# Optimization experiments

Hardware: AMD Instinct MI355X
Metric: run time of the kernel (lower is better)

Reference implementation:

```python
import jax, jax.numpy as jnp
import numpy as np

NUM_TOKENS = 16384
HIDDEN = 4096
NUM_EXPERTS = 256
TOP_K = 8
N_GROUP = 8
TOPK_GROUP = 4
NORM_TOPK_PROB = True
ROUTED_SCALING_FACTOR = 1.0


def setup_inputs() -> dict:
    key = jax.random.key(0)
    k1, k2, k3 = jax.random.split(key, 3)
    hidden_states = jax.random.normal(k1, (NUM_TOKENS, HIDDEN), dtype=jnp.float32)
    weight = jax.random.normal(k2, (NUM_EXPERTS, HIDDEN), dtype=jnp.float32) * (HIDDEN ** -0.5)
    e_score_correction_bias = jax.random.normal(k3, (NUM_EXPERTS,), dtype=jnp.float32) * 0.01
    return {"hidden_states": hidden_states, "weight": weight,
            "e_score_correction_bias": e_score_correction_bias}


def reference(hidden_states, weight, e_score_correction_bias):
    num_tokens = hidden_states.shape[0]
    # router logits: [T, E]
    logits = jnp.einsum('th,eh->te', hidden_states.astype(jnp.float32),
                        weight.astype(jnp.float32))
    scores = jax.nn.sigmoid(logits)
    scores_for_choice = scores + e_score_correction_bias[None, :]
    # group scores: sum of top-2 within each group, [T, G]
    per_group = scores_for_choice.reshape(num_tokens, N_GROUP, NUM_EXPERTS // N_GROUP)
    top2_vals, _ = jax.lax.top_k(per_group, 2)
    group_scores = top2_vals.sum(axis=-1)
    # select topk_group groups, build mask over experts
    _, group_idx = jax.lax.top_k(group_scores, TOPK_GROUP)  # [T, topk_group]
    group_mask = jnp.zeros_like(group_scores).at[
        jnp.arange(num_tokens)[:, None], group_idx].set(1.0)  # [T, G]
    score_mask = jnp.repeat(group_mask, NUM_EXPERTS // N_GROUP, axis=1)  # [T, E]
    tmp_scores = jnp.where(score_mask > 0, scores_for_choice, -jnp.inf)
    # final top-k experts over masked scores
    _, topk_idx = jax.lax.top_k(tmp_scores, TOP_K)  # [T, K]
    topk_weight = jnp.take_along_axis(scores, topk_idx, axis=1)
    if TOP_K > 1 and NORM_TOPK_PROB:
        denom = topk_weight.sum(axis=-1, keepdims=True) + 1e-20
        topk_weight = topk_weight / denom
    topk_weight = topk_weight * ROUTED_SCALING_FACTOR
    return logits, topk_weight, topk_idx
```

## Files before the change

### kernel.cpp

```cpp
#include <hip/hip_runtime.h>
#include <hip/hip_bf16.h>
#include <math.h>

#define TKN 16384
#define HID 4096
#define NE  256
#define TOPK 8
#define NGRP 8
#define TOPG 4

#define BM 128
#define BN 128
#define BKT 64
#define NKT (HID / BKT)

typedef _Float16 half8 __attribute__((ext_vector_type(8)));
typedef float    f32x4 __attribute__((ext_vector_type(4)));

static __device__ __forceinline__ unsigned pkrtz(float x, float y) {
    auto r = __builtin_amdgcn_cvt_pkrtz(x, y);
    return __builtin_bit_cast(unsigned, r);
}
static __device__ __forceinline__ float hi_mask(float a) {
    return __uint_as_float(__float_as_uint(a) & 0xFFFFE000u);
}

static __device__ __forceinline__ void split_store_16(
    const float4* p, unsigned char* hiPlane, unsigned char* loPlane,
    int srow, int skq)
{
    float e[16];
    #pragma unroll
    for (int i = 0; i < 4; ++i) {
        e[i*4+0] = p[i].x; e[i*4+1] = p[i].y; e[i*4+2] = p[i].z; e[i*4+3] = p[i].w;
    }
    unsigned hw[8], lw[8];
    #pragma unroll
    for (int j = 0; j < 8; ++j) {
        const float x0 = e[2*j], x1 = e[2*j+1];
        const float h0 = hi_mask(x0), h1 = hi_mask(x1);
        hw[j] = pkrtz(h0, h1);
        lw[j] = pkrtz(x0 - h0, x1 - h1);
    }
    #pragma unroll
    for (int c = 0; c < 2; ++c) {
        const int ad = srow * 128 + (((skq * 2) + c * 16) ^ ((srow & 7) << 4));
        *(uint4*)&hiPlane[ad] = make_uint4(hw[c*4+0], hw[c*4+1], hw[c*4+2], hw[c*4+3]);
        *(uint4*)&loPlane[ad] = make_uint4(lw[c*4+0], lw[c*4+1], lw[c*4+2], lw[c*4+3]);
    }
}

__global__ __launch_bounds__(512, 2) void gemm_split_f16(
    const float* __restrict__ A, const float* __restrict__ Bw, float* __restrict__ C)
{
    __shared__ __align__(16) unsigned char smem[2][4][BM * BKT * 2];

    const int tid  = threadIdx.x;
    const int lane = tid & 63;
    const int wave = tid >> 6;
    const int wg   = wave >> 2;
    const int wr   = (wave >> 1) & 1;
    const int wc   = wave & 1;

    const int row0 = blockIdx.y * BM;
    const int col0 = blockIdx.x * BN;

    const int srow = tid >> 2;
    const int skq  = (tid & 3) * 16;

    const float* aG = A  + (size_t)(row0 + srow) * HID + skq;
    const float* bG = Bw + (size_t)(col0 + srow) * HID + skq;

    f32x4 acc[16];
    #pragma unroll
    for (int i = 0; i < 16; ++i) acc[i] = (f32x4)0.f;

    float4 pa[4], pb[4];

    #pragma unroll
    for (int i = 0; i < 4; ++i) {
        pa[i] = *(const float4*)(aG + i * 4);
        pb[i] = *(const float4*)(bG + i * 4);
    }
    split_store_16(pa, &smem[0][0][0], &smem[0][1][0], srow, skq);
    split_store_16(pb, &smem[0][2][0], &smem[0][3][0], srow, skq);
    __syncthreads();

    for (int kt = 0; kt < NKT; ++kt) {
        const int cur = kt & 1;

        if (kt + 1 < NKT) {
            const float* ap = aG + (size_t)(kt + 1) * BKT;
            const float* bp = bG + (size_t)(kt + 1) * BKT;
            #pragma unroll
            for (int i = 0; i < 4; ++i) {
                pa[i] = *(const float4*)(ap + i * 4);
                pb[i] = *(const float4*)(bp + i * 4);
            }
        }

        {
            const int kbyte = wg * 64 + ((lane >> 4) << 4);
            half8 af[4][2], bf[4][2];
            #pragma unroll
            for (int mt = 0; mt < 4; ++mt) {
                const int m  = wr * 64 + mt * 16 + (lane & 15);
                const int ad = m * 128 + (kbyte ^ ((m & 7) << 4));
                af[mt][0] = *(const half8*)&smem[cur][0][ad];
                af[mt][1] = *(const half8*)&smem[cur][1][ad];
            }
            #pragma unroll
            for (int nt = 0; nt < 4; ++nt) {
                const int n  = wc * 64 + nt * 16 + (lane & 15);
                const int ad = n * 128 + (kbyte ^ ((n & 7) << 4));
                bf[nt][0] = *(const half8*)&smem[cur][2][ad];
                bf[nt][1] = *(const half8*)&smem[cur][3][ad];
            }
            #pragma unroll
            for (int mt = 0; mt < 4; ++mt)
                #pragma unroll
                for (int nt = 0; nt < 4; ++nt) {
                    f32x4 c = acc[mt*4+nt];
                    c = __builtin_amdgcn_mfma_f32_16x16x32_f16(af[mt][0], bf[nt][0], c, 0, 0, 0);
                    c = __builtin_amdgcn_mfma_f32_16x16x32_f16(af[mt][0], bf[nt][1], c, 0, 0, 0);
                    c = __builtin_amdgcn_mfma_f32_16x16x32_f16(af[mt][1], bf[nt][0], c, 0, 0, 0);
                    acc[mt*4+nt] = c;
                }
        }

        if (kt + 1 < NKT) {
            const int nb = (kt + 1) & 1;
            split_store_16(pa, &smem[nb][0][0], &smem[nb][1][0], srow, skq);
            split_store_16(pb, &smem[nb][2][0], &smem[nb][3][0], srow, skq);
        }
        __syncthreads();
    }

    __syncthreads();
    unsigned char* red = &smem[0][0][0];
    const int rbase = (wr * 2 + wc) * 16384;
    if (wg == 1) {
        #pragma unroll
        for (int f = 0; f < 16; ++f) {
            const int ad = rbase + ((lane * 256 + f * 16) ^ ((lane & 7) << 4));
            *(f32x4*)&red[ad] = acc[f];
        }
    }
    __syncthreads();
    if (wg == 0) {
        #pragma unroll
        for (int mt = 0; mt < 4; ++mt) {
            #pragma unroll
            for (int nt = 0; nt < 4; ++nt) {
                const int f  = mt * 4 + nt;
                const int ad = rbase + ((lane * 256 + f * 16) ^ ((lane & 7) << 4));
                f32x4 o = acc[f] + *(const f32x4*)&red[ad];
                const int r0 = row0 + wr * 64 + mt * 16 + ((lane >> 4) << 2);
                const int cc = col0 + wc * 64 + nt * 16 + (lane & 15);
                #pragma unroll
                for (int r = 0; r < 4; ++r)
                    C[(size_t)(r0 + r) * NE + cc] = o[r];
            }
        }
    }
}

__global__ __launch_bounds__(256) void router_topk_kernel(
    const float* __restrict__ logits, const float* __restrict__ bias,
    float* __restrict__ out_w, float* __restrict__ out_i)
{
    const int wid  = threadIdx.x >> 6;
    const int lane = threadIdx.x & 63;
    const int token = blockIdx.x * 4 + wid;

    const float* row = logits + (size_t)token * NE;
    const float4 lg = *(const float4*)&row[lane * 4];

    float sig[4], sc[4];
    {
        const float l4[4] = {lg.x, lg.y, lg.z, lg.w};
        #pragma unroll
        for (int j = 0; j < 4; ++j) {
            sig[j] = 1.f / (1.f + expf(-l4[j]));
            sc[j]  = sig[j] + bias[lane * 4 + j];
        }
    }

    float m1 = sc[0], m2 = -INFINITY;
    #pragma unroll
    for (int j = 1; j < 4; ++j) {
        if (sc[j] > m1) { m2 = m1; m1 = sc[j]; }
        else if (sc[j] > m2) { m2 = sc[j]; }
    }
    #pragma unroll
    for (int off = 1; off < 8; off <<= 1) {
        const float o1 = __shfl_xor(m1, off);
        const float o2 = __shfl_xor(m2, off);
        const float lo = fminf(m1, o1);
        m1 = fmaxf(m1, o1);
        m2 = fmaxf(lo, fmaxf(m2, o2));
    }
    const float gscore = m1 + m2;

    const int gmy = lane >> 3;
    int rank = 0;
    #pragma unroll
    for (int g = 0; g < NGRP; ++g) {
        const float gs = __shfl(gscore, g * 8);
        if (gs > gscore || (gs == gscore && g < gmy)) ++rank;
    }
    if (rank >= TOPG) {
        #pragma unroll
        for (int j = 0; j < 4; ++j) sc[j] = -INFINITY;
    }

    float wk[TOPK]; int ik[TOPK];
    float wsum = 0.f;
    #pragma unroll
    for (int k = 0; k < TOPK; ++k) {
        float bv = sc[0]; int bi = lane * 4;
        #pragma unroll
        for (int j = 1; j < 4; ++j)
            if (sc[j] > bv) { bv = sc[j]; bi = lane * 4 + j; }
        #pragma unroll
        for (int off = 1; off < 64; off <<= 1) {
            const float v2 = __shfl_xor(bv, off);
            const int   i2 = __shfl_xor(bi, off);
            if (v2 > bv || (v2 == bv && i2 < bi)) { bv = v2; bi = i2; }
        }
        const int owner = bi >> 2;
        const int j = bi & 3;
        const float sv = (j == 0) ? sig[0] : (j == 1) ? sig[1] : (j == 2) ? sig[2] : sig[3];
        const float w = __shfl(sv, owner);
        wk[k] = w; ik[k] = bi; wsum += w;
        if (lane == owner) {
            if (j == 0) sc[0] = -INFINITY;
            else if (j == 1) sc[1] = -INFINITY;
            else if (j == 2) sc[2] = -INFINITY;
            else sc[3] = -INFINITY;
        }
    }

    if (lane == 0) {
        const float denom = wsum + 1e-20f;
        #pragma unroll
        for (int k = 0; k < TOPK; ++k) {
            out_w[(size_t)token * TOPK + k] = wk[k] / denom;
            out_i[(size_t)token * TOPK + k] = (float)ik[k];
        }
    }
}

extern "C" void kernel_launch(void* const* d_in, const int* in_sizes, int n_in,
                              void* d_out, int out_size, void* d_ws, size_t ws_size,
                              hipStream_t stream) {
    const float* hidden = (const float*)d_in[0];
    const float* weight = (const float*)d_in[1];
    const float* bias   = (const float*)d_in[2];

    float* logits = (float*)d_out;
    float* out_w  = logits + (size_t)TKN * NE;
    float* out_i  = out_w + (size_t)TKN * TOPK;

    dim3 ggrid(NE / BN, TKN / BM);
    gemm_split_f16<<<ggrid, 512, 0, stream>>>(hidden, weight, logits);

    router_topk_kernel<<<TKN / 4, 256, 0, stream>>>(logits, bias, out_w, out_i);
}
```

Before: 186.3 us.

## Pre-split weight into f16 hi/lo tiles and restructure GEMM to 1024-thread blocks

Adds a prep kernel that converts the expert weight matrix once per call into pre-swizzled f16 hi/lo tile images in workspace, so the GEMM copies B tiles directly into LDS instead of converting them per block. The GEMM now uses 1024-thread blocks (16 waves, split-K over two wave groups), a padded A layout, and a block-index remap so paired column blocks share A rows. This removes redundant B conversion work across the 128 row blocks. It costs an extra launch and workspace traffic, and a 1024-thread block with heavy LDS use may limit occupancy.

```diff
diff --git a/kernel.cpp b/kernel.cpp
--- a/kernel.cpp
+++ b/kernel.cpp
@@ -11,8 +11,13 @@
 
 #define BM 128
 #define BN 128
-#define BKT 64
-#define NKT (HID / BKT)
+#define BK 64
+#define NKT (HID / BK)
+
+#define ASTR 144
+#define APL  (BM * ASTR)
+#define BPL  (BN * 128)
+#define BIMG (2 * BPL)
 
 typedef _Float16 half8 __attribute__((ext_vector_type(8)));
 typedef float    f32x4 __attribute__((ext_vector_type(4)));
@@ -25,138 +30,164 @@
     return __uint_as_float(__float_as_uint(a) & 0xFFFFE000u);
 }
 
-static __device__ __forceinline__ void split_store_16(
-    const float4* p, unsigned char* hiPlane, unsigned char* loPlane,
-    int srow, int skq)
+__global__ __launch_bounds__(256) void prep_b(const float* __restrict__ B,
+                                              unsigned char* __restrict__ ws)
 {
-    float e[16];
-    #pragma unroll
-    for (int i = 0; i < 4; ++i) {
-        e[i*4+0] = p[i].x; e[i*4+1] = p[i].y; e[i*4+2] = p[i].z; e[i*4+3] = p[i].w;
-    }
-    unsigned hw[8], lw[8];
-    #pragma unroll
-    for (int j = 0; j < 8; ++j) {
-        const float x0 = e[2*j], x1 = e[2*j+1];
+    const int gid = blockIdx.x * 256 + threadIdx.x;
+    const int e   = gid >> 9;
+    const int k0  = (gid & 511) * 8;
+    const float* src = B + (size_t)e * HID + k0;
+    float v[8];
+    #pragma unroll
+    for (int i = 0; i < 8; ++i) v[i] = src[i];
+    unsigned hw[4], lw[4];
+    #pragma unroll
+    for (int j = 0; j < 4; ++j) {
+        const float x0 = v[2*j], x1 = v[2*j+1];
         const float h0 = hi_mask(x0), h1 = hi_mask(x1);
         hw[j] = pkrtz(h0, h1);
         lw[j] = pkrtz(x0 - h0, x1 - h1);
     }
-    #pragma unroll
-    for (int c = 0; c < 2; ++c) {
-        const int ad = srow * 128 + (((skq * 2) + c * 16) ^ ((srow & 7) << 4));
-        *(uint4*)&hiPlane[ad] = make_uint4(hw[c*4+0], hw[c*4+1], hw[c*4+2], hw[c*4+3]);
-        *(uint4*)&loPlane[ad] = make_uint4(lw[c*4+0], lw[c*4+1], lw[c*4+2], lw[c*4+3]);
-    }
-}
-
-__global__ __launch_bounds__(512, 2) void gemm_split_f16(
-    const float* __restrict__ A, const float* __restrict__ Bw, float* __restrict__ C)
+    const int cb  = e >> 7;
+    const int row = e & 127;
+    const int kt  = k0 >> 6;
+    const int x   = ((k0 & 63) * 2) ^ ((row & 7) << 4);
+    unsigned char* img = ws + (size_t)(cb * NKT + kt) * BIMG + row * 128 + x;
+    *(uint4*)(img)       = make_uint4(hw[0], hw[1], hw[2], hw[3]);
+    *(uint4*)(img + BPL) = make_uint4(lw[0], lw[1], lw[2], lw[3]);
+}
+
+__global__ __launch_bounds__(1024, 4) void gemm_mfma(
+    const float* __restrict__ A, const unsigned char* __restrict__ Bws,
+    float* __restrict__ C)
 {
-    __shared__ __align__(16) unsigned char smem[2][4][BM * BKT * 2];
+    __shared__ __align__(16) unsigned char sA[2][2][APL];
+    __shared__ __align__(16) unsigned char sB[2][BIMG];
 
     const int tid  = threadIdx.x;
     const int lane = tid & 63;
     const int wave = tid >> 6;
-    const int wg   = wave >> 2;
-    const int wr   = (wave >> 1) & 1;
-    const int wc   = wave & 1;
-
-    const int row0 = blockIdx.y * BM;
-    const int col0 = blockIdx.x * BN;
-
-    const int srow = tid >> 2;
-    const int skq  = (tid & 3) * 16;
-
-    const float* aG = A  + (size_t)(row0 + srow) * HID + skq;
-    const float* bG = Bw + (size_t)(col0 + srow) * HID + skq;
-
-    f32x4 acc[16];
-    #pragma unroll
-    for (int i = 0; i < 16; ++i) acc[i] = (f32x4)0.f;
-
-    float4 pa[4], pb[4];
-
-    #pragma unroll
-    for (int i = 0; i < 4; ++i) {
-        pa[i] = *(const float4*)(aG + i * 4);
-        pb[i] = *(const float4*)(bG + i * 4);
-    }
-    split_store_16(pa, &smem[0][0][0], &smem[0][1][0], srow, skq);
-    split_store_16(pb, &smem[0][2][0], &smem[0][3][0], srow, skq);
+    const int wg = wave >> 3;
+    const int wr = (wave >> 2) & 1;
+    const int wc = wave & 3;
+
+    const int bid  = blockIdx.x;
+    const int mb   = (bid & 7) * 16 + (bid >> 4);
+    const int cb   = (bid >> 3) & 1;
+    const int row0 = mb * BM;
+
+    const int arow = tid >> 4;
+    const int acol = (tid & 15) * 4;
+    const float* aG0 = A + (size_t)(row0 + arow) * HID + acol;
+    const float* aG1 = aG0 + (size_t)64 * HID;
+    const int aw0 = arow * ASTR + acol * 2;
+    const int aw1 = (arow + 64) * ASTR + acol * 2;
+
+    const unsigned char* bG = Bws + (size_t)cb * NKT * BIMG + tid * 16;
+    const int bw0 = tid * 16, bw1 = 16384 + tid * 16;
+
+    const int afr = wr * 64 + (lane & 15);
+    const int afo = afr * ASTR + (wg * 4 + (lane >> 4)) * 16;
+    const int bfr = wc * 32 + (lane & 15);
+    const int bfx = (wg * 4 + (lane >> 4)) * 16;
+
+    f32x4 acc[4][2];
+    #pragma unroll
+    for (int i = 0; i < 4; ++i) { acc[i][0] = (f32x4)0.f; acc[i][1] = (f32x4)0.f; }
+
+    float4 av0, av1; uint4 bv0, bv1;
+
+    av0 = *(const float4*)(aG0);
+    av1 = *(const float4*)(aG1);
+    bv0 = *(const uint4*)(bG);
+    bv1 = *(const uint4*)(bG + 16384);
+    {
+        const float h0 = hi_mask(av0.x), h1 = hi_mask(av0.y),
+                    h2 = hi_mask(av0.z), h3 = hi_mask(av0.w);
+        *(uint2*)&sA[0][0][aw0] = make_uint2(pkrtz(h0, h1), pkrtz(h2, h3));
+        *(uint2*)&sA[0][1][aw0] = make_uint2(pkrtz(av0.x - h0, av0.y - h1),
+                                             pkrtz(av0.z - h2, av0.w - h3));
+        const float g0 = hi_mask(av1.x), g1 = hi_mask(av1.y),
+                    g2 = hi_mask(av1.z), g3 = hi_mask(av1.w);
+        *(uint2*)&sA[0][0][aw1] = make_uint2(pkrtz(g0, g1), pkrtz(g2, g3));
+        *(uint2*)&sA[0][1][aw1] = make_uint2(pkrtz(av1.x - g0, av1.y - g1),
+                                             pkrtz(av1.z - g2, av1.w - g3));
+        *(uint4*)&sB[0][bw0] = bv0;
+        *(uint4*)&sB[0][bw1] = bv1;
+    }
     __syncthreads();
 
     for (int kt = 0; kt < NKT; ++kt) {
         const int cur = kt & 1;
-
-        if (kt + 1 < NKT) {
-            const float* ap = aG + (size_t)(kt + 1) * BKT;
-            const float* bp = bG + (size_t)(kt + 1) * BKT;
+        const bool more = (kt + 1 < NKT);
+        if (more) {
+            av0 = *(const float4*)(aG0 + (kt + 1) * BK);
+            av1 = *(const float4*)(aG1 + (kt + 1) * BK);
+            const unsigned char* bp = bG + (size_t)(kt + 1) * BIMG;
+            bv0 = *(const uint4*)(bp);
+            bv1 = *(const uint4*)(bp + 16384);
+        }
+        {
+            half8 bf[2][2];
             #pragma unroll
-            for (int i = 0; i < 4; ++i) {
-                pa[i] = *(const float4*)(ap + i * 4);
-                pb[i] = *(const float4*)(bp + i * 4);
+            for (int nt = 0; nt < 2; ++nt) {
+                const int r  = bfr + nt * 16;
+                const int ad = r * 128 + (bfx ^ ((r & 7) << 4));
+                bf[nt][0] = *(const half8*)&sB[cur][ad];
+                bf[nt][1] = *(const half8*)&sB[cur][BPL + ad];
             }
-        }
-
-        {
-            const int kbyte = wg * 64 + ((lane >> 4) << 4);
-            half8 af[4][2], bf[4][2];
             #pragma unroll
             for (int mt = 0; mt < 4; ++mt) {
-                const int m  = wr * 64 + mt * 16 + (lane & 15);
-                const int ad = m * 128 + (kbyte ^ ((m & 7) << 4));
-                af[mt][0] = *(const half8*)&smem[cur][0][ad];
-                af[mt][1] = *(const half8*)&smem[cur][1][ad];
+                const int ad = afo + mt * 16 * ASTR;
+                const half8 ah = *(const half8*)&sA[cur][0][ad];
+                const half8 al = *(const half8*)&sA[cur][1][ad];
+                #pragma unroll
+                for (int nt = 0; nt < 2; ++nt) {
+                    f32x4 c = acc[mt][nt];
+                    c = __builtin_amdgcn_mfma_f32_16x16x32_f16(ah, bf[nt][0], c, 0, 0, 0);
+                    c = __builtin_amdgcn_mfma_f32_16x16x32_f16(ah, bf[nt][1], c, 0, 0, 0);
+                    c = __builtin_amdgcn_mfma_f32_16x16x32_f16(al, bf[nt][0], c, 0, 0, 0);
+                    acc[mt][nt] = c;
+                }
             }
+        }
+        if (more) {
+            const int nb = cur ^ 1;
+            const float h0 = hi_mask(av0.x), h1 = hi_mask(av0.y),
+                        h2 = hi_mask(av0.z), h3 = hi_mask(av0.w);
+            *(uint2*)&sA[nb][0][aw0] = make_uint2(pkrtz(h0, h1), pkrtz(h2, h3));
+            *(uint2*)&sA[nb][1][aw0] = make_uint2(pkrtz(av0.x - h0, av0.y - h1),
+                                                  pkrtz(av0.z - h2, av0.w - h3));
+            const float g0 = hi_mask(av1.x), g1 = hi_mask(av1.y),
+                        g2 = hi_mask(av1.z), g3 = hi_mask(av1.w);
+            *(uint2*)&sA[nb][0][aw1] = make_uint2(pkrtz(g0, g1), pkrtz(g2, g3));
+            *(uint2*)&sA[nb][1][aw1] = make_uint2(pkrtz(av1.x - g0, av1.y - g1),
+                                                  pkrtz(av1.z - g2, av1.w - g3));
+            *(uint4*)&sB[nb][bw0] = bv0;
+            *(uint4*)&sB[nb][bw1] = bv1;
+        }
+        __syncthreads();
+    }
+
+    unsigned char* red = &sA[0][0][0];
+    const int fbase = (wave & 7) * 8192;
+    if (wg == 1) {
+        #pragma unroll
+        for (int mt = 0; mt < 4; ++mt)
             #pragma unroll
-            for (int nt = 0; nt < 4; ++nt) {
-                const int n  = wc * 64 + nt * 16 + (lane & 15);
-                const int ad = n * 128 + (kbyte ^ ((n & 7) << 4));
-                bf[nt][0] = *(const half8*)&smem[cur][2][ad];
-                bf[nt][1] = *(const half8*)&smem[cur][3][ad];
-            }
-            #pragma unroll
-            for (int mt = 0; mt < 4; ++mt)
-                #pragma unroll
-                for (int nt = 0; nt < 4; ++nt) {
-                    f32x4 c = acc[mt*4+nt];
-                    c = __builtin_amdgcn_mfma_f32_16x16x32_f16(af[mt][0], bf[nt][0], c, 0, 0, 0);
-                    c = __builtin_amdgcn_mfma_f32_16x16x32_f16(af[mt][0], bf[nt][1], c, 0, 0, 0);
-                    c = __builtin_amdgcn_mfma_f32_16x16x32_f16(af[mt][1], bf[nt][0], c, 0, 0, 0);
-                    acc[mt*4+nt] = c;
-                }
-        }
-
-        if (kt + 1 < NKT) {
-            const int nb = (kt + 1) & 1;
-            split_store_16(pa, &smem[nb][0][0], &smem[nb][1][0], srow, skq);
-            split_store_16(pb, &smem[nb][2][0], &smem[nb][3][0], srow, skq);
-        }
-        __syncthreads();
-    }
-
-    __syncthreads();
-    unsigned char* red = &smem[0][0][0];
-    const int rbase = (wr * 2 + wc) * 16384;
-    if (wg == 1) {
-        #pragma unroll
-        for (int f = 0; f < 16; ++f) {
-            const int ad = rbase + ((lane * 256 + f * 16) ^ ((lane & 7) << 4));
-            *(f32x4*)&red[ad] = acc[f];
-        }
+            for (int nt = 0; nt < 2; ++nt)
+                *(f32x4*)&red[fbase + (mt * 2 + nt) * 1024 + lane * 16] = acc[mt][nt];
     }
     __syncthreads();
     if (wg == 0) {
         #pragma unroll
         for (int mt = 0; mt < 4; ++mt) {
             #pragma unroll
-            for (int nt = 0; nt < 4; ++nt) {
-                const int f  = mt * 4 + nt;
-                const int ad = rbase + ((lane * 256 + f * 16) ^ ((lane & 7) << 4));
-                f32x4 o = acc[f] + *(const f32x4*)&red[ad];
-                const int r0 = row0 + wr * 64 + mt * 16 + ((lane >> 4) << 2);
-                const int cc = col0 + wc * 64 + nt * 16 + (lane & 15);
+            for (int nt = 0; nt < 2; ++nt) {
+                f32x4 o = acc[mt][nt] +
+                          *(const f32x4*)&red[fbase + (mt * 2 + nt) * 1024 + lane * 16];
+                const int r0 = row0 + wr * 64 + mt * 16 + (lane >> 4) * 4;
+                const int cc = cb * 128 + wc * 32 + nt * 16 + (lane & 15);
                 #pragma unroll
                 for (int r = 0; r < 4; ++r)
                     C[(size_t)(r0 + r) * NE + cc] = o[r];
@@ -262,8 +293,9 @@
     float* out_w  = logits + (size_t)TKN * NE;
     float* out_i  = out_w + (size_t)TKN * TOPK;
 
-    dim3 ggrid(NE / BN, TKN / BM);
-    gemm_split_f16<<<ggrid, 512, 0, stream>>>(hidden, weight, logits);
-
+    unsigned char* bpl = (unsigned char*)d_ws;
+
+    prep_b<<<512, 256, 0, stream>>>(weight, bpl);
+    gemm_mfma<<<256, 1024, 0, stream>>>(hidden, bpl, logits);
     router_topk_kernel<<<TKN / 4, 256, 0, stream>>>(logits, bias, out_w, out_i);
 }
```

Result: faster. 150.1 us (-19.5%).
